# Performance work log

Measured on AMD Instinct MI355X. Metric: run time of the kernel, lower is better.

## Reference

```python
import jax, jax.numpy as jnp
import numpy as np
from jax import lax

B, F, N, C = 1024, 256, 65536, 1000
SOURCE_CLASSES = 751
TEMP = 0.05
MOMENTUM = 0.2


def setup_inputs() -> dict:
    key = jax.random.key(0)
    k1, k2, k3, k4 = jax.random.split(key, 4)
    inputs = jax.random.normal(k1, (B, F), dtype=jnp.float32)
    # indexes in [1, N] so that (indexes - 1) are all valid -> the boolean mask
    # `inds = indexes >= 0` keeps every row (static shapes under jit)
    indexes = jax.random.randint(k2, (B,), 1, N + 1, dtype=jnp.int32)
    features = jax.random.normal(k3, (N, F), dtype=jnp.float32)
    features = features / jnp.linalg.norm(features, axis=1, keepdims=True)  # bank stores unit rows
    labels = jax.random.randint(k4, (N,), 0, C, dtype=jnp.int32)
    return {"inputs": inputs, "indexes": indexes, "features": features, "labels": labels}


def _forward(inputs, idx, features, labels):
    # F.normalize(inputs, dim=1)
    x = inputs / jnp.linalg.norm(inputs, axis=1, keepdims=True)           # [B, F]
    logits = (x @ features.T) / TEMP                                      # [B, N]
    targets = labels[idx]                                                 # [B]
    # sim.index_add_(0, labels, inputs.t()) -> per-class column sums
    sim = jax.ops.segment_sum(logits.T, labels, num_segments=C)           # [C, B]
    nums = jax.ops.segment_sum(jnp.ones((N,), jnp.float32), labels, num_segments=C)  # [C]
    mask = nums > 0
    sim = sim / jnp.where(mask, nums, 1.0)[:, None]                       # per-class mean
    # masked softmax over classes (faithful to original: plain exp, +eps denominator)
    exps = jnp.exp(sim.T) * mask[None, :].astype(jnp.float32)            # [B, C]
    p = exps / (exps.sum(axis=1, keepdims=True) + 1e-6)
    logp = jnp.log(p + 1e-6)
    # F.nll_loss(..., ignore_index=source_classes-1)
    valid = (targets != SOURCE_CLASSES - 1).astype(jnp.float32)
    nll = -jnp.take_along_axis(logp, targets[:, None], axis=1)[:, 0]
    loss = jnp.sum(nll * valid) / jnp.maximum(valid.sum(), 1.0)
    return loss, x


def reference(inputs, indexes, features, labels):
    idx = indexes - 1
    idx = jnp.where(idx == 5554, SOURCE_CLASSES - 1, idx)  # is_source=True special case
    loss, x = _forward(inputs, idx, features, labels)
    # HM.backward's per-sample sequential momentum scatter update + renorm of the bank.
    # Order-dependent on duplicate indices -> inherently sequential -> lax.scan.
    def step(feats, xy):
        xi, yi = xy
        row = MOMENTUM * feats[yi] + (1.0 - MOMENTUM) * xi
        row = row / jnp.linalg.norm(row)
        return feats.at[yi].set(row), None

    new_features, _ = lax.scan(step, features, (x, idx))
    return loss, new_features
```

## Files before the change

### kernel.cpp

```cpp
#include <hip/hip_runtime.h>
#include <math.h>

#define Bn   1024
#define Fdim 256
#define Nn   65536
#define Cn   1000
#define INV_TEMP 20.0f
#define MOM  0.2f

struct WS {
  float x[Bn * Fdim];
  float meanP[Fdim * Cn];
  float mask[Cn];
  float sumExp[Bn];
  float tExp[Bn];
  int   idx[Bn];
  int   targets[Bn];
  int   counts[Cn];
  int   offsets[Cn];
  int   cursor[Cn];
  int   list[Nn];
};

__global__ void k0_zero(int* __restrict__ counts, float* __restrict__ sumExp) {
  int t = blockIdx.x * blockDim.x + threadIdx.x;
  if (t < Cn) counts[t] = 0;
  if (t < Bn) sumExp[t] = 0.f;
}

__global__ __launch_bounds__(64) void k1_norm(const float* __restrict__ inputs,
                                              const int* __restrict__ indexes,
                                              const int* __restrict__ labels,
                                              float* __restrict__ x,
                                              int* __restrict__ idx, int* __restrict__ targets) {
  int b = blockIdx.x, t = threadIdx.x;
  float4 v = *(const float4*)&inputs[b * Fdim + t * 4];
  float s = v.x * v.x + v.y * v.y + v.z * v.z + v.w * v.w;
#pragma unroll
  for (int o = 32; o > 0; o >>= 1) s += __shfl_xor(s, o, 64);
  float inv = 1.0f / sqrtf(s);
  v.x *= inv; v.y *= inv; v.z *= inv; v.w *= inv;
  *(float4*)&x[b * Fdim + t * 4] = v;
  if (t == 0) {
    int i0 = indexes[b] - 1;
    if (i0 == 5554) i0 = 750;
    idx[b] = i0;
    targets[b] = labels[i0];
  }
}

__global__ void k2_count(const int* __restrict__ labels, int* __restrict__ counts) {
  int n = blockIdx.x * blockDim.x + threadIdx.x;
  atomicAdd(&counts[labels[n]], 1);
}

__global__ void k3_scan(const int* __restrict__ counts, int* __restrict__ offsets,
                        int* __restrict__ cursor) {
  __shared__ int s[1024];
  int t = threadIdx.x;
  int v = (t < Cn) ? counts[t] : 0;
  s[t] = v;
  __syncthreads();
  for (int o = 1; o < 1024; o <<= 1) {
    int a = (t >= o) ? s[t - o] : 0;
    __syncthreads();
    s[t] += a;
    __syncthreads();
  }
  if (t < Cn) {
    int off = s[t] - v;
    offsets[t] = off;
    cursor[t] = off;
  }
}

__global__ void k4_fill(const int* __restrict__ labels, int* __restrict__ cursor,
                        int* __restrict__ list) {
  int n = blockIdx.x * blockDim.x + threadIdx.x;
  int c = labels[n];
  int p = atomicAdd(&cursor[c], 1);
  list[p] = n;
}

__global__ __launch_bounds__(512) void k5_classsum(const float* __restrict__ features,
                                                   const int* __restrict__ list,
                                                   const int* __restrict__ offsets,
                                                   const int* __restrict__ counts,
                                                   float* __restrict__ meanP,
                                                   float* __restrict__ mask,
                                                   float* __restrict__ out1) {
  int c = blockIdx.x, t = threadIdx.x, w = t >> 6, lane = t & 63;
  int off = offsets[c], cnt = counts[c];
  __shared__ int mlds[512];
  __shared__ float partial[8][256];
  float4 acc = {0.f, 0.f, 0.f, 0.f};
  for (int base = 0; base < cnt; base += 512) {
    int m = min(512, cnt - base);
    if (t < m) mlds[t] = list[off + base + t];
    __syncthreads();
    int i = w;
    for (; i + 8 < m; i += 16) {
      int n0 = mlds[i], n1 = mlds[i + 8];
      float4 v0 = *(const float4*)&features[n0 * Fdim + lane * 4];
      float4 v1 = *(const float4*)&features[n1 * Fdim + lane * 4];
      acc.x += v0.x + v1.x; acc.y += v0.y + v1.y;
      acc.z += v0.z + v1.z; acc.w += v0.w + v1.w;
      float* o0 = &out1[n0 * Fdim + lane * 4];
      o0[0] = v0.x; o0[1] = v0.y; o0[2] = v0.z; o0[3] = v0.w;
      float* o1 = &out1[n1 * Fdim + lane * 4];
      o1[0] = v1.x; o1[1] = v1.y; o1[2] = v1.z; o1[3] = v1.w;
    }
    for (; i < m; i += 8) {
      int n = mlds[i];
      float4 v = *(const float4*)&features[n * Fdim + lane * 4];
      acc.x += v.x; acc.y += v.y; acc.z += v.z; acc.w += v.w;
      float* o = &out1[n * Fdim + lane * 4];
      o[0] = v.x; o[1] = v.y; o[2] = v.z; o[3] = v.w;
    }
    __syncthreads();
  }
  *(float4*)&partial[w][lane * 4] = acc;
  __syncthreads();
  if (t < 256) {
    float s = 0.f;
#pragma unroll
    for (int ww = 0; ww < 8; ww++) s += partial[ww][t];
    meanP[((t >> 2) * Cn + c) * 4 + (t & 3)] = (cnt > 0) ? s / (float)cnt : 0.f;
    if (t == 0) mask[c] = (cnt > 0) ? 1.f : 0.f;
  }
}

#define BBT 8
__global__ __launch_bounds__(256) void k6_matmul(const float* __restrict__ x,
                                                 const float* __restrict__ meanP,
                                                 const float* __restrict__ mask,
                                                 const int* __restrict__ targets,
                                                 float* __restrict__ sumExp,
                                                 float* __restrict__ tExp) {
  int b0 = blockIdx.x * BBT;
  int c  = blockIdx.y * 256 + threadIdx.x;
  int lane = threadIdx.x & 63;
  bool cv = (c < Cn);
  int cc = cv ? c : 0;
  float acc[BBT];
#pragma unroll
  for (int bb = 0; bb < BBT; bb++) acc[bb] = 0.f;
  const float* xb = x + b0 * Fdim;
#pragma unroll 4
  for (int f4 = 0; f4 < Fdim / 4; f4++) {
    float4 mv = *(const float4*)&meanP[(f4 * Cn + cc) * 4];
#pragma unroll
    for (int bb = 0; bb < BBT; bb++) {
      float4 xv = *(const float4*)&xb[bb * Fdim + f4 * 4];
      acc[bb] = fmaf(xv.x, mv.x, acc[bb]);
      acc[bb] = fmaf(xv.y, mv.y, acc[bb]);
      acc[bb] = fmaf(xv.z, mv.z, acc[bb]);
      acc[bb] = fmaf(xv.w, mv.w, acc[bb]);
    }
  }
  float msk = cv ? mask[cc] : 0.f;
#pragma unroll
  for (int bb = 0; bb < BBT; bb++) {
    float e = msk * __expf(acc[bb] * INV_TEMP);
    float s = e;
#pragma unroll
    for (int o = 32; o > 0; o >>= 1) s += __shfl_down(s, o, 64);
    if (lane == 0) atomicAdd(&sumExp[b0 + bb], s);
    int tgt = targets[b0 + bb];
    if (cv && tgt == c) tExp[b0 + bb] = e;
  }
}

__global__ void k7_loss(const float* __restrict__ sumExp, const float* __restrict__ tExp,
                        const int* __restrict__ targets, float* __restrict__ out) {
  int t = threadIdx.x;
  float S = sumExp[t], tE = tExp[t];
  float nll = -logf(tE / (S + 1e-6f) + 1e-6f);
  float valid = (targets[t] != 750) ? 1.f : 0.f;
  float a = nll * valid, b = valid;
#pragma unroll
  for (int o = 32; o > 0; o >>= 1) {
    a += __shfl_down(a, o, 64);
    b += __shfl_down(b, o, 64);
  }
  __shared__ float ra[16], rb[16];
  if ((t & 63) == 0) { ra[t >> 6] = a; rb[t >> 6] = b; }
  __syncthreads();
  if (t == 0) {
    float sa = 0.f, sb = 0.f;
    for (int i = 0; i < 16; i++) { sa += ra[i]; sb += rb[i]; }
    out[0] = sa / fmaxf(sb, 1.f);
  }
}

__global__ __launch_bounds__(256) void k8_update(const float* __restrict__ features,
                                                 const float* __restrict__ x,
                                                 const int* __restrict__ idx,
                                                 float* __restrict__ out1) {
  __shared__ int ilds[Bn];
  int t = threadIdx.x;
  for (int i = t; i < Bn; i += 256) ilds[i] = idx[i];
  __syncthreads();
  int wid = t >> 6, lane = t & 63;
  int b = blockIdx.x * 4 + wid;
  int y = ilds[b];
  for (int base = 0; base < b; base += 64) {
    int j = base + lane;
    bool hit = (j < b) && (ilds[j] == y);
    if (__any(hit)) return;
  }
  float4 r = *(const float4*)&features[y * Fdim + lane * 4];
  for (int base = (b >> 6) << 6; base < Bn; base += 64) {
    int k = base + lane;
    bool hit = (k >= b) && (ilds[k] == y);
    unsigned long long mbits = __ballot(hit);
    while (mbits) {
      int p = __ffsll(mbits) - 1;
      mbits &= mbits - 1;
      int kk = base + p;
      float4 xv = *(const float4*)&x[kk * Fdim + lane * 4];
      r.x = MOM * r.x + (1.f - MOM) * xv.x;
      r.y = MOM * r.y + (1.f - MOM) * xv.y;
      r.z = MOM * r.z + (1.f - MOM) * xv.z;
      r.w = MOM * r.w + (1.f - MOM) * xv.w;
      float ss = r.x * r.x + r.y * r.y + r.z * r.z + r.w * r.w;
#pragma unroll
      for (int o = 32; o > 0; o >>= 1) ss += __shfl_xor(ss, o, 64);
      float inv = 1.0f / sqrtf(ss);
      r.x *= inv; r.y *= inv; r.z *= inv; r.w *= inv;
    }
  }
  int base2 = y * Fdim + lane * 4;
  out1[base2 + 0] = r.x;
  out1[base2 + 1] = r.y;
  out1[base2 + 2] = r.z;
  out1[base2 + 3] = r.w;
}

extern "C" void kernel_launch(void* const* d_in, const int* in_sizes, int n_in,
                              void* d_out, int out_size, void* d_ws, size_t ws_size,
                              hipStream_t stream) {
  const float* inputs   = (const float*)d_in[0];
  const int*   indexes  = (const int*)d_in[1];
  const float* features = (const float*)d_in[2];
  const int*   labels   = (const int*)d_in[3];
  float* out = (float*)d_out;
  WS* w = (WS*)d_ws;

  k0_zero<<<4, 256, 0, stream>>>(w->counts, w->sumExp);
  k1_norm<<<Bn, 64, 0, stream>>>(inputs, indexes, labels, w->x, w->idx, w->targets);
  k2_count<<<Nn / 256, 256, 0, stream>>>(labels, w->counts);
  k3_scan<<<1, 1024, 0, stream>>>(w->counts, w->offsets, w->cursor);
  k4_fill<<<Nn / 256, 256, 0, stream>>>(labels, w->cursor, w->list);
  k5_classsum<<<Cn, 512, 0, stream>>>(features, w->list, w->offsets, w->counts,
                                      w->meanP, w->mask, out + 1);
  k6_matmul<<<dim3(Bn / BBT, 4), 256, 0, stream>>>(w->x, w->meanP, w->mask, w->targets,
                                                   w->sumExp, w->tExp);
  k7_loss<<<1, 1024, 0, stream>>>(w->sumExp, w->tExp, w->targets, out);
  k8_update<<<Bn / 4, 256, 0, stream>>>(features, w->x, w->idx, out + 1);
}
```

Baseline: 213.6 us.

## Fuse zeroing and loss kernels, vectorize label passes, shrink block sizes

```diff
diff --git a/kernel.cpp b/kernel.cpp
--- a/kernel.cpp
+++ b/kernel.cpp
@@ -22,18 +22,17 @@
   int   list[Nn];
 };
 
-__global__ void k0_zero(int* __restrict__ counts, float* __restrict__ sumExp) {
-  int t = blockIdx.x * blockDim.x + threadIdx.x;
-  if (t < Cn) counts[t] = 0;
-  if (t < Bn) sumExp[t] = 0.f;
-}
-
 __global__ __launch_bounds__(64) void k1_norm(const float* __restrict__ inputs,
                                               const int* __restrict__ indexes,
                                               const int* __restrict__ labels,
                                               float* __restrict__ x,
-                                              int* __restrict__ idx, int* __restrict__ targets) {
+                                              int* __restrict__ idx, int* __restrict__ targets,
+                                              int* __restrict__ counts,
+                                              float* __restrict__ sumExp) {
   int b = blockIdx.x, t = threadIdx.x;
+  int g = b * 64 + t;
+  if (g < Cn) counts[g] = 0;
+  if (g < Bn) sumExp[g] = 0.f;
   float4 v = *(const float4*)&inputs[b * Fdim + t * 4];
   float s = v.x * v.x + v.y * v.y + v.z * v.z + v.w * v.w;
 #pragma unroll
@@ -49,9 +48,14 @@
   }
 }
 
-__global__ void k2_count(const int* __restrict__ labels, int* __restrict__ counts) {
-  int n = blockIdx.x * blockDim.x + threadIdx.x;
-  atomicAdd(&counts[labels[n]], 1);
+__global__ __launch_bounds__(256) void k2_count(const int* __restrict__ labels,
+                                                int* __restrict__ counts) {
+  int t = blockIdx.x * blockDim.x + threadIdx.x;
+  int4 l = *(const int4*)&labels[t * 4];
+  atomicAdd(&counts[l.x], 1);
+  atomicAdd(&counts[l.y], 1);
+  atomicAdd(&counts[l.z], 1);
+  atomicAdd(&counts[l.w], 1);
 }
 
 __global__ void k3_scan(const int* __restrict__ counts, int* __restrict__ offsets,
@@ -74,15 +78,19 @@
   }
 }
 
-__global__ void k4_fill(const int* __restrict__ labels, int* __restrict__ cursor,
-                        int* __restrict__ list) {
-  int n = blockIdx.x * blockDim.x + threadIdx.x;
-  int c = labels[n];
-  int p = atomicAdd(&cursor[c], 1);
-  list[p] = n;
-}
-
-__global__ __launch_bounds__(512) void k5_classsum(const float* __restrict__ features,
+__global__ __launch_bounds__(256) void k4_fill(const int* __restrict__ labels,
+                                               int* __restrict__ cursor,
+                                               int* __restrict__ list) {
+  int t = blockIdx.x * blockDim.x + threadIdx.x;
+  int4 l = *(const int4*)&labels[t * 4];
+  int n = t * 4;
+  list[atomicAdd(&cursor[l.x], 1)] = n;
+  list[atomicAdd(&cursor[l.y], 1)] = n + 1;
+  list[atomicAdd(&cursor[l.z], 1)] = n + 2;
+  list[atomicAdd(&cursor[l.w], 1)] = n + 3;
+}
+
+__global__ __launch_bounds__(256) void k5_classsum(const float* __restrict__ features,
                                                    const int* __restrict__ list,
                                                    const int* __restrict__ offsets,
                                                    const int* __restrict__ counts,
@@ -92,15 +100,15 @@
   int c = blockIdx.x, t = threadIdx.x, w = t >> 6, lane = t & 63;
   int off = offsets[c], cnt = counts[c];
   __shared__ int mlds[512];
-  __shared__ float partial[8][256];
+  __shared__ float partial[4][256];
   float4 acc = {0.f, 0.f, 0.f, 0.f};
   for (int base = 0; base < cnt; base += 512) {
     int m = min(512, cnt - base);
-    if (t < m) mlds[t] = list[off + base + t];
+    for (int i = t; i < m; i += 256) mlds[i] = list[off + base + i];
     __syncthreads();
     int i = w;
-    for (; i + 8 < m; i += 16) {
-      int n0 = mlds[i], n1 = mlds[i + 8];
+    for (; i + 4 < m; i += 8) {
+      int n0 = mlds[i], n1 = mlds[i + 4];
       float4 v0 = *(const float4*)&features[n0 * Fdim + lane * 4];
       float4 v1 = *(const float4*)&features[n1 * Fdim + lane * 4];
       acc.x += v0.x + v1.x; acc.y += v0.y + v1.y;
@@ -110,7 +118,7 @@
       float* o1 = &out1[n1 * Fdim + lane * 4];
       o1[0] = v1.x; o1[1] = v1.y; o1[2] = v1.z; o1[3] = v1.w;
     }
-    for (; i < m; i += 8) {
+    for (; i < m; i += 4) {
       int n = mlds[i];
       float4 v = *(const float4*)&features[n * Fdim + lane * 4];
       acc.x += v.x; acc.y += v.y; acc.z += v.z; acc.w += v.w;
@@ -121,16 +129,12 @@
   }
   *(float4*)&partial[w][lane * 4] = acc;
   __syncthreads();
-  if (t < 256) {
-    float s = 0.f;
-#pragma unroll
-    for (int ww = 0; ww < 8; ww++) s += partial[ww][t];
-    meanP[((t >> 2) * Cn + c) * 4 + (t & 3)] = (cnt > 0) ? s / (float)cnt : 0.f;
-    if (t == 0) mask[c] = (cnt > 0) ? 1.f : 0.f;
-  }
-}
-
-#define BBT 8
+  float s = partial[0][t] + partial[1][t] + partial[2][t] + partial[3][t];
+  meanP[((t >> 2) * Cn + c) * 4 + (t & 3)] = (cnt > 0) ? s / (float)cnt : 0.f;
+  if (t == 0) mask[c] = (cnt > 0) ? 1.f : 0.f;
+}
+
+#define BBT 4
 __global__ __launch_bounds__(256) void k6_matmul(const float* __restrict__ x,
                                                  const float* __restrict__ meanP,
                                                  const float* __restrict__ mask,
@@ -171,34 +175,41 @@
   }
 }
 
-__global__ void k7_loss(const float* __restrict__ sumExp, const float* __restrict__ tExp,
-                        const int* __restrict__ targets, float* __restrict__ out) {
-  int t = threadIdx.x;
-  float S = sumExp[t], tE = tExp[t];
-  float nll = -logf(tE / (S + 1e-6f) + 1e-6f);
-  float valid = (targets[t] != 750) ? 1.f : 0.f;
-  float a = nll * valid, b = valid;
-#pragma unroll
-  for (int o = 32; o > 0; o >>= 1) {
-    a += __shfl_down(a, o, 64);
-    b += __shfl_down(b, o, 64);
-  }
-  __shared__ float ra[16], rb[16];
-  if ((t & 63) == 0) { ra[t >> 6] = a; rb[t >> 6] = b; }
-  __syncthreads();
-  if (t == 0) {
-    float sa = 0.f, sb = 0.f;
-    for (int i = 0; i < 16; i++) { sa += ra[i]; sb += rb[i]; }
-    out[0] = sa / fmaxf(sb, 1.f);
-  }
-}
-
 __global__ __launch_bounds__(256) void k8_update(const float* __restrict__ features,
                                                  const float* __restrict__ x,
                                                  const int* __restrict__ idx,
+                                                 const float* __restrict__ sumExp,
+                                                 const float* __restrict__ tExp,
+                                                 const int* __restrict__ targets,
+                                                 float* __restrict__ out,
                                                  float* __restrict__ out1) {
+  int t = threadIdx.x;
+  if (blockIdx.x == 256) {
+    float a = 0.f, bsum = 0.f;
+#pragma unroll
+    for (int k = 0; k < 4; k++) {
+      int b = t + k * 256;
+      float S = sumExp[b], tE = tExp[b];
+      float nll = -logf(tE / (S + 1e-6f) + 1e-6f);
+      float valid = (targets[b] != 750) ? 1.f : 0.f;
+      a += nll * valid; bsum += valid;
+    }
+#pragma unroll
+    for (int o = 32; o > 0; o >>= 1) {
+      a += __shfl_down(a, o, 64);
+      bsum += __shfl_down(bsum, o, 64);
+    }
+    __shared__ float ra[4], rb[4];
+    if ((t & 63) == 0) { ra[t >> 6] = a; rb[t >> 6] = bsum; }
+    __syncthreads();
+    if (t == 0) {
+      float sa = ra[0] + ra[1] + ra[2] + ra[3];
+      float sb = rb[0] + rb[1] + rb[2] + rb[3];
+      out[0] = sa / fmaxf(sb, 1.f);
+    }
+    return;
+  }
   __shared__ int ilds[Bn];
-  int t = threadIdx.x;
   for (int i = t; i < Bn; i += 256) ilds[i] = idx[i];
   __syncthreads();
   int wid = t >> 6, lane = t & 63;
@@ -247,15 +258,15 @@
   float* out = (float*)d_out;
   WS* w = (WS*)d_ws;
 
-  k0_zero<<<4, 256, 0, stream>>>(w->counts, w->sumExp);
-  k1_norm<<<Bn, 64, 0, stream>>>(inputs, indexes, labels, w->x, w->idx, w->targets);
-  k2_count<<<Nn / 256, 256, 0, stream>>>(labels, w->counts);
+  k1_norm<<<Bn, 64, 0, stream>>>(inputs, indexes, labels, w->x, w->idx, w->targets,
+                                 w->counts, w->sumExp);
+  k2_count<<<Nn / 1024, 256, 0, stream>>>(labels, w->counts);
   k3_scan<<<1, 1024, 0, stream>>>(w->counts, w->offsets, w->cursor);
-  k4_fill<<<Nn / 256, 256, 0, stream>>>(labels, w->cursor, w->list);
-  k5_classsum<<<Cn, 512, 0, stream>>>(features, w->list, w->offsets, w->counts,
+  k4_fill<<<Nn / 1024, 256, 0, stream>>>(labels, w->cursor, w->list);
+  k5_classsum<<<Cn, 256, 0, stream>>>(features, w->list, w->offsets, w->counts,
                                       w->meanP, w->mask, out + 1);
   k6_matmul<<<dim3(Bn / BBT, 4), 256, 0, stream>>>(w->x, w->meanP, w->mask, w->targets,
                                                    w->sumExp, w->tExp);
-  k7_loss<<<1, 1024, 0, stream>>>(w->sumExp, w->tExp, w->targets, out);
-  k8_update<<<Bn / 4, 256, 0, stream>>>(features, w->x, w->idx, out + 1);
-}
+  k8_update<<<Bn / 4 + 1, 256, 0, stream>>>(features, w->x, w->idx, w->sumExp, w->tExp,
+                                            w->targets, out, out + 1);
+}
```

Result: faster. 198.6 us (-7.0%).
